# Kernel tuning notes

Hardware: AMD Instinct MI355X
Metric: run time of the kernel (lower is better)

## Reference

```python
import jax, jax.numpy as jnp
import numpy as np
from jax import lax


def _binarize(w):
    # XNOR-style sign binarization: sign(w) with sign(0) -> +1
    return jnp.where(w >= 0, 1.0, -1.0).astype(w.dtype)


def setup_inputs() -> dict:
    key = jax.random.key(0)
    kx, kw = jax.random.split(key)
    X = jax.random.normal(kx, (32, 256, 56, 56), dtype=jnp.float32)   # NCHW
    W = jax.random.normal(kw, (256, 256, 3, 3), dtype=jnp.float32)    # OIHW
    return {"X": X, "W": W}


def reference(X, W):
    Wb = _binarize(W)
    # F.conv2d default: padding=0 (VALID), stride=1
    out = lax.conv_general_dilated(
        X, Wb,
        window_strides=(1, 1),
        padding="VALID",
        dimension_numbers=("NCHW", "OIHW", "NCHW"),
    )
    return out  # [32, 256, 54, 54]
```

## Files before the change

kernel.cpp:

```cpp
#include <hip/hip_runtime.h>
#include <stdint.h>

typedef float f32x4 __attribute__((ext_vector_type(4)));
typedef __bf16 bf16x8 __attribute__((ext_vector_type(8)));
typedef unsigned short u16x8 __attribute__((ext_vector_type(8)));

#define NIMG 32
#define CIN  256
#define HWIN 3136
#define COUT 256
#define HWOUT 2916
#define NPOS 93312

#define XT_BYTES   ((size_t)NIMG*HWIN*CIN*2)
#define WT_OFF     (XT_BYTES + 8192)
#define WT_BYTES   ((size_t)9*4*2*128*64*2)
#define WS_NEED    (WT_OFF + WT_BYTES)

static __device__ __forceinline__ unsigned short f2bf(float f) {
    union { float f; uint32_t u; } v; v.f = f;
    return (unsigned short)((v.u + 0x7FFFu + ((v.u >> 16) & 1u)) >> 16);
}

static __device__ __forceinline__ void gload16(const void* g, void* l) {
    __builtin_amdgcn_global_load_lds(
        (const __attribute__((address_space(1))) void*)g,
        (__attribute__((address_space(3))) void*)l, 16, 0, 0);
}

static __device__ __forceinline__ uint32_t lds_a(const void* p) {
    return (uint32_t)(uintptr_t)(__attribute__((address_space(3))) const void*)p;
}

static __device__ __forceinline__ u16x8 ldsr(uint32_t addr) {
    u16x8 r;
    asm volatile("ds_read_b128 %0, %1" : "=v"(r) : "v"(addr));
    return r;
}

#define BAR()   __builtin_amdgcn_s_barrier()
#define LGKM0() do { asm volatile("s_waitcnt lgkmcnt(0)" ::: "memory"); \
                     __builtin_amdgcn_sched_barrier(0); } while (0)
#define VM2()   asm volatile("s_waitcnt vmcnt(2)" ::: "memory")
#define VM6()   asm volatile("s_waitcnt vmcnt(6)" ::: "memory")
#define VM0()   asm volatile("s_waitcnt vmcnt(0)" ::: "memory")
#define PRIO1() __builtin_amdgcn_s_setprio(1)
#define PRIO0() __builtin_amdgcn_s_setprio(0)

#define MF(a_, b_, c_) __builtin_amdgcn_mfma_f32_16x16x32_bf16( \
    __builtin_bit_cast(bf16x8, a_), __builtin_bit_cast(bf16x8, b_), c_, 0, 0, 0)

#define QUAD(aa, ab, m0_, m1_, c0_, c1_, c2_, c3_)         \
    acc[m0_][0] = MF(aa, c0_, acc[m0_][0]);                \
    acc[m0_][1] = MF(aa, c1_, acc[m0_][1]);                \
    acc[m0_][2] = MF(aa, c2_, acc[m0_][2]);                \
    acc[m0_][3] = MF(aa, c3_, acc[m0_][3]);                \
    acc[m1_][0] = MF(ab, c0_, acc[m1_][0]);                \
    acc[m1_][1] = MF(ab, c1_, acc[m1_][1]);                \
    acc[m1_][2] = MF(ab, c2_, acc[m1_][2]);                \
    acc[m1_][3] = MF(ab, c3_, acc[m1_][3]);

__global__ void wxform(const float* __restrict__ W, unsigned short* __restrict__ Wt) {
    int idx = blockIdx.x * 256 + threadIdx.x;
    int c6 = idx & 63;
    int o7 = (idx >> 6) & 127;
    int ob = (idx >> 13) & 1;
    int cc = (idx >> 14) & 3;
    int k9 = idx >> 16;
    int o = ob * 128 + o7;
    int c = cc * 64 + c6;
    float w = W[(size_t)(o * 256 + c) * 9 + k9];
    Wt[idx] = (w >= 0.0f) ? (unsigned short)0x3F80 : (unsigned short)0xBF80;
}

__global__ void xxform(const float* __restrict__ X, unsigned short* __restrict__ Xt) {
    __shared__ float tile[32][65];
    int bid = blockIdx.x;
    int hwc = bid % 49;
    int cc  = (bid / 49) & 7;
    int n   = bid / (49 * 8);
    int hw0 = hwc * 64;
    int c0  = cc * 32;
    int t = threadIdx.x;
    {
        int c = t >> 3;
        int w = (t & 7) * 8;
        const float* src = X + (size_t)(n * CIN + c0 + c) * HWIN + hw0 + w;
        float4 a = *(const float4*)src;
        float4 b = *(const float4*)(src + 4);
        tile[c][w + 0] = a.x; tile[c][w + 1] = a.y; tile[c][w + 2] = a.z; tile[c][w + 3] = a.w;
        tile[c][w + 4] = b.x; tile[c][w + 5] = b.y; tile[c][w + 6] = b.z; tile[c][w + 7] = b.w;
    }
    __syncthreads();
    {
        int w  = t >> 2;
        int cb = (t & 3) * 8;
        u16x8 v;
        #pragma unroll
        for (int j = 0; j < 8; ++j) v[j] = f2bf(tile[cb + j][w]);
        *(u16x8*)(Xt + (size_t)(n * HWIN + hw0 + w) * 256 + c0 + cb) = v;
    }
}

__global__ __launch_bounds__(512, 2)
void bconv_gemm(const unsigned short* __restrict__ Xt,
                const unsigned short* __restrict__ Wt,
                float* __restrict__ out) {
    __shared__ __align__(16) char smem[98304];

    const int t    = threadIdx.x;
    const int wid  = t >> 6;
    const int lane = t & 63;
    const int l15  = lane & 15;
    const int lg   = lane >> 4;
    const int wr   = wid >> 2;
    const int wc   = wid & 3;
    const int ob   = blockIdx.x;
    const uint32_t P0 = blockIdx.y * 256u;

    const uint32_t colx = (uint32_t)(((t & 7) ^ ((t >> 3) & 7)) << 3);
    const uint32_t aG   = (uint32_t)(t >> 3) * 64u + colx;

    uint32_t base0[4];
    #pragma unroll
    for (int r = 0; r < 4; ++r) {
        uint32_t pos = P0 + (uint32_t)(r * 64 + (t >> 3));
        if (pos >= NPOS) pos = NPOS - 1;
        uint32_t ni = pos / (uint32_t)HWOUT;
        uint32_t rm = pos - ni * HWOUT;
        uint32_t ph = rm / 54u;
        uint32_t pw = rm - ph * 54u;
        base0[r] = ni * HWIN + ph * 56u + pw;
    }

    const uint32_t x7  = (uint32_t)(l15 & 7);
    const uint32_t ck0 = ((((uint32_t)lg) ^ x7) << 4);
    const uint32_t ck1 = (((4u | (uint32_t)lg) ^ x7) << 4);
    const uint32_t ar0 = (uint32_t)(wr * 64 + 0 * 16 + l15) * 128u;
    const uint32_t ar1 = (uint32_t)(wr * 64 + 1 * 16 + l15) * 128u;
    const uint32_t ar2 = (uint32_t)(wr * 64 + 2 * 16 + l15) * 128u;
    const uint32_t ar3 = (uint32_t)(wr * 64 + 3 * 16 + l15) * 128u;
    const uint32_t br0 = 16384u + (uint32_t)(wc * 64 + 0 * 16 + l15) * 128u;
    const uint32_t br1 = 16384u + (uint32_t)(wc * 64 + 1 * 16 + l15) * 128u;
    const uint32_t br2 = 16384u + (uint32_t)(wc * 64 + 2 * 16 + l15) * 128u;
    const uint32_t br3 = 16384u + (uint32_t)(wc * 64 + 3 * 16 + l15) * 128u;

    const uint32_t E = lds_a(smem);
    const uint32_t O = E + 49152u;

    f32x4 acc[4][4];
    #pragma unroll
    for (int m = 0; m < 4; ++m)
        #pragma unroll
        for (int n = 0; n < 4; ++n)
            acc[m][n] = (f32x4){0.f, 0.f, 0.f, 0.f};

    auto STAGE_A = [&](uint32_t bufoff, int kt) {
        int k9 = kt >> 2, cc = kt & 3;
        const unsigned short* p = Wt + ((size_t)(((k9 << 2) | cc) * 2 + ob)) * 8192 + aG;
        gload16(p,        smem + bufoff + (size_t)t * 16);
        gload16(p + 4096, smem + bufoff + 8192 + (size_t)t * 16);
    };
    auto STAGE_B2 = [&](uint32_t bufoff, int kt, int r0) {
        int k9 = kt >> 2, cc = kt & 3;
        int kh = k9 / 3, kw = k9 - kh * 3;
        uint32_t khw = (uint32_t)(kh * 56 + kw);
        #pragma unroll
        for (int r = r0; r < r0 + 2; ++r) {
            const unsigned short* p = Xt + (size_t)(base0[r] + khw) * 256 + (uint32_t)cc * 64u + colx;
            gload16(p, smem + bufoff + 16384 + (size_t)r * 8192 + (size_t)t * 16);
        }
    };

    STAGE_A(0, 0);      STAGE_B2(0, 0, 0);      STAGE_B2(0, 0, 2);
    STAGE_A(49152u, 1); STAGE_B2(49152u, 1, 0); STAGE_B2(49152u, 1, 2);
    VM6();
    BAR();

    u16x8 a00, a01, a10, a11;
    u16x8 b00, b10, b20, b30, b01, b11, b21, b31;

    auto ITER = [&](int kt, bool pf) {
        a00 = ldsr(E + ar0 + ck0); a01 = ldsr(E + ar0 + ck1);
        a10 = ldsr(E + ar1 + ck0); a11 = ldsr(E + ar1 + ck1);
        b00 = ldsr(E + br0 + ck0); b10 = ldsr(E + br1 + ck0);
        b20 = ldsr(E + br2 + ck0); b30 = ldsr(E + br3 + ck0);
        BAR(); LGKM0(); PRIO1();
        QUAD(a00, a10, 0, 1, b00, b10, b20, b30);
        PRIO0(); BAR();
        b01 = ldsr(E + br0 + ck1); b11 = ldsr(E + br1 + ck1);
        b21 = ldsr(E + br2 + ck1); b31 = ldsr(E + br3 + ck1);
        BAR(); LGKM0(); PRIO1();
        QUAD(a01, a11, 0, 1, b01, b11, b21, b31);
        PRIO0(); BAR();
        a00 = ldsr(E + ar2 + ck0); a01 = ldsr(E + ar2 + ck1);
        a10 = ldsr(E + ar3 + ck0); a11 = ldsr(E + ar3 + ck1);
        BAR(); LGKM0(); PRIO1();
        QUAD(a00, a10, 2, 3, b00, b10, b20, b30);
        PRIO0(); BAR();
        if (pf) { STAGE_A(0, kt + 2); VM2(); } else { VM0(); }
        BAR(); PRIO1();
        QUAD(a01, a11, 2, 3, b01, b11, b21, b31);
        PRIO0(); BAR();
        a00 = ldsr(O + ar0 + ck0); a01 = ldsr(O + ar0 + ck1);
        a10 = ldsr(O + ar1 + ck0); a11 = ldsr(O + ar1 + ck1);
        b00 = ldsr(O + br0 + ck0); b10 = ldsr(O + br1 + ck0);
        b20 = ldsr(O + br2 + ck0); b30 = ldsr(O + br3 + ck0);
        if (pf) STAGE_B2(0, kt + 2, 0);
        BAR(); LGKM0(); PRIO1();
        QUAD(a00, a10, 0, 1, b00, b10, b20, b30);
        PRIO0(); BAR();
        b01 = ldsr(O + br0 + ck1); b11 = ldsr(O + br1 + ck1);
        b21 = ldsr(O + br2 + ck1); b31 = ldsr(O + br3 + ck1);
        if (pf) STAGE_B2(0, kt + 2, 2);
        BAR(); LGKM0(); PRIO1();
        QUAD(a01, a11, 0, 1, b01, b11, b21, b31);
        PRIO0(); BAR();
        a00 = ldsr(O + ar2 + ck0); a01 = ldsr(O + ar2 + ck1);
        a10 = ldsr(O + ar3 + ck0); a11 = ldsr(O + ar3 + ck1);
        BAR(); LGKM0(); PRIO1();
        QUAD(a00, a10, 2, 3, b00, b10, b20, b30);
        PRIO0(); BAR();
        if (pf) {
            STAGE_A(49152u, kt + 3);
            STAGE_B2(49152u, kt + 3, 0);
            STAGE_B2(49152u, kt + 3, 2);
            VM6();
        } else {
            VM0();
        }
        BAR(); PRIO1();
        QUAD(a01, a11, 2, 3, b01, b11, b21, b31);
        PRIO0(); BAR();
    };

    for (int kt = 0; kt < 34; kt += 2) ITER(kt, true);
    ITER(34, false);

    const int orow0 = ob * 128 + wr * 64;
    #pragma unroll
    for (int n = 0; n < 4; ++n) {
        uint32_t P = P0 + (uint32_t)(wc * 64 + n * 16 + l15);
        if (P < NPOS) {
            uint32_t ni = P / (uint32_t)HWOUT;
            uint32_t rm = P - ni * HWOUT;
            float* ob_ = out + (size_t)(ni * 256u + orow0) * HWOUT + rm;
            #pragma unroll
            for (int m = 0; m < 4; ++m)
                #pragma unroll
                for (int r = 0; r < 4; ++r)
                    ob_[(size_t)(m * 16 + lg * 4 + r) * HWOUT] = acc[m][n][r];
        }
    }
}

__global__ void bconv_fallback(const float* __restrict__ X, const float* __restrict__ W,
                               float* __restrict__ out) {
    size_t idx = (size_t)blockIdx.x * 256 + threadIdx.x;
    int ow = (int)(idx % 54);
    int oh = (int)((idx / 54) % 54);
    int o  = (int)((idx / 2916) % 256);
    int n  = (int)(idx / 746496);
    float s = 0.f;
    for (int c = 0; c < 256; ++c) {
        const float* xr = X + ((size_t)(n * 256 + c) * 56 + oh) * 56 + ow;
        const float* wr = W + (size_t)(o * 256 + c) * 9;
        #pragma unroll
        for (int kh = 0; kh < 3; ++kh)
            #pragma unroll
            for (int kw = 0; kw < 3; ++kw) {
                float w = wr[kh * 3 + kw];
                float x = xr[kh * 56 + kw];
                s += (w >= 0.f) ? x : -x;
            }
    }
    out[idx] = s;
}

extern "C" void kernel_launch(void* const* d_in, const int* in_sizes, int n_in,
                              void* d_out, int out_size, void* d_ws, size_t ws_size,
                              hipStream_t stream) {
    const float* X = (const float*)d_in[0];
    const float* W = (const float*)d_in[1];
    float* out = (float*)d_out;

    if (ws_size < WS_NEED) {
        bconv_fallback<<<93312, 256, 0, stream>>>(X, W, out);
        return;
    }
    unsigned short* Xt = (unsigned short*)d_ws;
    unsigned short* Wt = (unsigned short*)((char*)d_ws + WT_OFF);

    wxform<<<2304, 256, 0, stream>>>(W, Wt);
    xxform<<<12544, 256, 0, stream>>>(X, Xt);

    dim3 grid(2, 365);
    bconv_gemm<<<grid, 512, 0, stream>>>(Xt, Wt, out);
}
```

Measured before the change: 163.4 us.

## Shrink GEMM block to 128x128 with 4 waves and K-chunk 64

The implicit-GEMM kernel moves from 512-thread blocks on a 128x256 tile to 256-thread blocks on a 128x128 tile, which doubles the grid and lowers LDS use to 64 KB. The inner loop changes from split half-K QUADs to full 16-MFMA steps with 8 fragment reads per step. B addresses are precomputed as byte pointers advanced by an incremental koff. Bounds checks are dropped because NPOS divides evenly by 128. The cost is less reuse per block, more global traffic for the A and B tiles, and a waitcnt schedule that has been changed.

```diff
diff --git a/kernel.cpp b/kernel.cpp
--- a/kernel.cpp
+++ b/kernel.cpp
@@ -14,7 +14,7 @@
 
 #define XT_BYTES   ((size_t)NIMG*HWIN*CIN*2)
 #define WT_OFF     (XT_BYTES + 8192)
-#define WT_BYTES   ((size_t)9*4*2*128*64*2)
+#define WT_BYTES   ((size_t)36*2*128*64*2)
 #define WS_NEED    (WT_OFF + WT_BYTES)
 
 static __device__ __forceinline__ unsigned short f2bf(float f) {
@@ -41,8 +41,7 @@
 #define BAR()   __builtin_amdgcn_s_barrier()
 #define LGKM0() do { asm volatile("s_waitcnt lgkmcnt(0)" ::: "memory"); \
                      __builtin_amdgcn_sched_barrier(0); } while (0)
-#define VM2()   asm volatile("s_waitcnt vmcnt(2)" ::: "memory")
-#define VM6()   asm volatile("s_waitcnt vmcnt(6)" ::: "memory")
+#define VM8()   asm volatile("s_waitcnt vmcnt(8)" ::: "memory")
 #define VM0()   asm volatile("s_waitcnt vmcnt(0)" ::: "memory")
 #define PRIO1() __builtin_amdgcn_s_setprio(1)
 #define PRIO0() __builtin_amdgcn_s_setprio(0)
@@ -50,15 +49,23 @@
 #define MF(a_, b_, c_) __builtin_amdgcn_mfma_f32_16x16x32_bf16( \
     __builtin_bit_cast(bf16x8, a_), __builtin_bit_cast(bf16x8, b_), c_, 0, 0, 0)
 
-#define QUAD(aa, ab, m0_, m1_, c0_, c1_, c2_, c3_)         \
-    acc[m0_][0] = MF(aa, c0_, acc[m0_][0]);                \
-    acc[m0_][1] = MF(aa, c1_, acc[m0_][1]);                \
-    acc[m0_][2] = MF(aa, c2_, acc[m0_][2]);                \
-    acc[m0_][3] = MF(aa, c3_, acc[m0_][3]);                \
-    acc[m1_][0] = MF(ab, c0_, acc[m1_][0]);                \
-    acc[m1_][1] = MF(ab, c1_, acc[m1_][1]);                \
-    acc[m1_][2] = MF(ab, c2_, acc[m1_][2]);                \
-    acc[m1_][3] = MF(ab, c3_, acc[m1_][3]);
+#define M16()                                              \
+    acc[0][0] = MF(a0, b0, acc[0][0]);                     \
+    acc[1][0] = MF(a1, b0, acc[1][0]);                     \
+    acc[2][0] = MF(a2, b0, acc[2][0]);                     \
+    acc[3][0] = MF(a3, b0, acc[3][0]);                     \
+    acc[0][1] = MF(a0, b1, acc[0][1]);                     \
+    acc[1][1] = MF(a1, b1, acc[1][1]);                     \
+    acc[2][1] = MF(a2, b1, acc[2][1]);                     \
+    acc[3][1] = MF(a3, b1, acc[3][1]);                     \
+    acc[0][2] = MF(a0, b2, acc[0][2]);                     \
+    acc[1][2] = MF(a1, b2, acc[1][2]);                     \
+    acc[2][2] = MF(a2, b2, acc[2][2]);                     \
+    acc[3][2] = MF(a3, b2, acc[3][2]);                     \
+    acc[0][3] = MF(a0, b3, acc[0][3]);                     \
+    acc[1][3] = MF(a1, b3, acc[1][3]);                     \
+    acc[2][3] = MF(a2, b3, acc[2][3]);                     \
+    acc[3][3] = MF(a3, b3, acc[3][3]);
 
 __global__ void wxform(const float* __restrict__ W, unsigned short* __restrict__ Wt) {
     int idx = blockIdx.x * 256 + threadIdx.x;
@@ -102,35 +109,36 @@
     }
 }
 
-__global__ __launch_bounds__(512, 2)
+__global__ __launch_bounds__(256, 2)
 void bconv_gemm(const unsigned short* __restrict__ Xt,
                 const unsigned short* __restrict__ Wt,
                 float* __restrict__ out) {
-    __shared__ __align__(16) char smem[98304];
+    __shared__ __align__(16) char smem[65536];
 
     const int t    = threadIdx.x;
     const int wid  = t >> 6;
     const int lane = t & 63;
     const int l15  = lane & 15;
     const int lg   = lane >> 4;
-    const int wr   = wid >> 2;
-    const int wc   = wid & 3;
+    const int wr   = wid >> 1;
+    const int wc   = wid & 1;
     const int ob   = blockIdx.x;
-    const uint32_t P0 = blockIdx.y * 256u;
-
-    const uint32_t colx = (uint32_t)(((t & 7) ^ ((t >> 3) & 7)) << 3);
-    const uint32_t aG   = (uint32_t)(t >> 3) * 64u + colx;
-
-    uint32_t base0[4];
+    const uint32_t P0 = blockIdx.y * 128u;
+
+    const uint32_t colxB = (uint32_t)(((t & 7) ^ ((t >> 3) & 7)) << 4);
+    const uint32_t rowt  = (uint32_t)(t >> 3);
+
+    const char* pA0 = (const char*)Wt + (size_t)ob * 16384 + rowt * 128 + colxB;
+
+    const char* bB[4];
     #pragma unroll
     for (int r = 0; r < 4; ++r) {
-        uint32_t pos = P0 + (uint32_t)(r * 64 + (t >> 3));
-        if (pos >= NPOS) pos = NPOS - 1;
+        uint32_t pos = P0 + (uint32_t)(r * 32) + rowt;
         uint32_t ni = pos / (uint32_t)HWOUT;
         uint32_t rm = pos - ni * HWOUT;
         uint32_t ph = rm / 54u;
         uint32_t pw = rm - ph * 54u;
-        base0[r] = ni * HWIN + ph * 56u + pw;
+        bB[r] = (const char*)Xt + (size_t)(ni * HWIN + ph * 56u + pw) * 512 + colxB;
     }
 
     const uint32_t x7  = (uint32_t)(l15 & 7);
@@ -146,7 +154,7 @@
     const uint32_t br3 = 16384u + (uint32_t)(wc * 64 + 3 * 16 + l15) * 128u;
 
     const uint32_t E = lds_a(smem);
-    const uint32_t O = E + 49152u;
+    const uint32_t O = E + 32768u;
 
     f32x4 acc[4][4];
     #pragma unroll
@@ -156,82 +164,68 @@
             acc[m][n] = (f32x4){0.f, 0.f, 0.f, 0.f};
 
     auto STAGE_A = [&](uint32_t bufoff, int kt) {
-        int k9 = kt >> 2, cc = kt & 3;
-        const unsigned short* p = Wt + ((size_t)(((k9 << 2) | cc) * 2 + ob)) * 8192 + aG;
-        gload16(p,        smem + bufoff + (size_t)t * 16);
-        gload16(p + 4096, smem + bufoff + 8192 + (size_t)t * 16);
-    };
-    auto STAGE_B2 = [&](uint32_t bufoff, int kt, int r0) {
-        int k9 = kt >> 2, cc = kt & 3;
-        int kh = k9 / 3, kw = k9 - kh * 3;
-        uint32_t khw = (uint32_t)(kh * 56 + kw);
-        #pragma unroll
-        for (int r = r0; r < r0 + 2; ++r) {
-            const unsigned short* p = Xt + (size_t)(base0[r] + khw) * 256 + (uint32_t)cc * 64u + colx;
-            gload16(p, smem + bufoff + 16384 + (size_t)r * 8192 + (size_t)t * 16);
+        const char* p = pA0 + (uint32_t)kt * 32768u;
+        #pragma unroll
+        for (int r = 0; r < 4; ++r)
+            gload16(p + r * 4096, smem + bufoff + r * 4096 + (size_t)t * 16);
+    };
+    auto STAGE_B = [&](uint32_t bufoff, uint32_t koff) {
+        #pragma unroll
+        for (int r = 0; r < 4; ++r)
+            gload16(bB[r] + koff, smem + bufoff + 16384 + r * 4096 + (size_t)t * 16);
+    };
+
+    uint32_t ccE = 2, k3E = 0, koffE = 256;
+    uint32_t ccO = 3, k3O = 0, koffO = 384;
+    auto adv2 = [](uint32_t& cc, uint32_t& k3, uint32_t& koff) {
+        #pragma unroll
+        for (int s = 0; s < 2; ++s) {
+            if (cc == 3) { cc = 0; koff += ((k3 == 2) ? 54u : 1u) * 512u - 384u; k3 = (k3 == 2) ? 0u : k3 + 1u; }
+            else         { cc++; koff += 128u; }
         }
     };
 
-    STAGE_A(0, 0);      STAGE_B2(0, 0, 0);      STAGE_B2(0, 0, 2);
-    STAGE_A(49152u, 1); STAGE_B2(49152u, 1, 0); STAGE_B2(49152u, 1, 2);
-    VM6();
+    STAGE_A(0, 0);      STAGE_B(0, 0);
+    STAGE_A(32768u, 1); STAGE_B(32768u, 128);
+    VM8();
     BAR();
 
-    u16x8 a00, a01, a10, a11;
-    u16x8 b00, b10, b20, b30, b01, b11, b21, b31;
+    u16x8 a0, a1, a2, a3, b0, b1, b2, b3;
 
     auto ITER = [&](int kt, bool pf) {
-        a00 = ldsr(E + ar0 + ck0); a01 = ldsr(E + ar0 + ck1);
-        a10 = ldsr(E + ar1 + ck0); a11 = ldsr(E + ar1 + ck1);
-        b00 = ldsr(E + br0 + ck0); b10 = ldsr(E + br1 + ck0);
-        b20 = ldsr(E + br2 + ck0); b30 = ldsr(E + br3 + ck0);
-        BAR(); LGKM0(); PRIO1();
-        QUAD(a00, a10, 0, 1, b00, b10, b20, b30);
-        PRIO0(); BAR();
-        b01 = ldsr(E + br0 + ck1); b11 = ldsr(E + br1 + ck1);
-        b21 = ldsr(E + br2 + ck1); b31 = ldsr(E + br3 + ck1);
-        BAR(); LGKM0(); PRIO1();
-        QUAD(a01, a11, 0, 1, b01, b11, b21, b31);
-        PRIO0(); BAR();
-        a00 = ldsr(E + ar2 + ck0); a01 = ldsr(E + ar2 + ck1);
-        a10 = ldsr(E + ar3 + ck0); a11 = ldsr(E + ar3 + ck1);
-        BAR(); LGKM0(); PRIO1();
-        QUAD(a00, a10, 2, 3, b00, b10, b20, b30);
-        PRIO0(); BAR();
-        if (pf) { STAGE_A(0, kt + 2); VM2(); } else { VM0(); }
-        BAR(); PRIO1();
-        QUAD(a01, a11, 2, 3, b01, b11, b21, b31);
-        PRIO0(); BAR();
-        a00 = ldsr(O + ar0 + ck0); a01 = ldsr(O + ar0 + ck1);
-        a10 = ldsr(O + ar1 + ck0); a11 = ldsr(O + ar1 + ck1);
-        b00 = ldsr(O + br0 + ck0); b10 = ldsr(O + br1 + ck0);
-        b20 = ldsr(O + br2 + ck0); b30 = ldsr(O + br3 + ck0);
-        if (pf) STAGE_B2(0, kt + 2, 0);
-        BAR(); LGKM0(); PRIO1();
-        QUAD(a00, a10, 0, 1, b00, b10, b20, b30);
-        PRIO0(); BAR();
-        b01 = ldsr(O + br0 + ck1); b11 = ldsr(O + br1 + ck1);
-        b21 = ldsr(O + br2 + ck1); b31 = ldsr(O + br3 + ck1);
-        if (pf) STAGE_B2(0, kt + 2, 2);
-        BAR(); LGKM0(); PRIO1();
-        QUAD(a01, a11, 0, 1, b01, b11, b21, b31);
-        PRIO0(); BAR();
-        a00 = ldsr(O + ar2 + ck0); a01 = ldsr(O + ar2 + ck1);
-        a10 = ldsr(O + ar3 + ck0); a11 = ldsr(O + ar3 + ck1);
-        BAR(); LGKM0(); PRIO1();
-        QUAD(a00, a10, 2, 3, b00, b10, b20, b30);
-        PRIO0(); BAR();
-        if (pf) {
-            STAGE_A(49152u, kt + 3);
-            STAGE_B2(49152u, kt + 3, 0);
-            STAGE_B2(49152u, kt + 3, 2);
-            VM6();
-        } else {
-            VM0();
-        }
-        BAR(); PRIO1();
-        QUAD(a01, a11, 2, 3, b01, b11, b21, b31);
-        PRIO0(); BAR();
+        a0 = ldsr(E + ar0 + ck0); a1 = ldsr(E + ar1 + ck0);
+        a2 = ldsr(E + ar2 + ck0); a3 = ldsr(E + ar3 + ck0);
+        b0 = ldsr(E + br0 + ck0); b1 = ldsr(E + br1 + ck0);
+        b2 = ldsr(E + br2 + ck0); b3 = ldsr(E + br3 + ck0);
+        BAR(); LGKM0(); PRIO1();
+        M16();
+        PRIO0(); BAR();
+        a0 = ldsr(E + ar0 + ck1); a1 = ldsr(E + ar1 + ck1);
+        a2 = ldsr(E + ar2 + ck1); a3 = ldsr(E + ar3 + ck1);
+        b0 = ldsr(E + br0 + ck1); b1 = ldsr(E + br1 + ck1);
+        b2 = ldsr(E + br2 + ck1); b3 = ldsr(E + br3 + ck1);
+        VM0();
+        BAR(); LGKM0(); PRIO1();
+        M16();
+        PRIO0(); BAR();
+        a0 = ldsr(O + ar0 + ck0); a1 = ldsr(O + ar1 + ck0);
+        a2 = ldsr(O + ar2 + ck0); a3 = ldsr(O + ar3 + ck0);
+        b0 = ldsr(O + br0 + ck0); b1 = ldsr(O + br1 + ck0);
+        b2 = ldsr(O + br2 + ck0); b3 = ldsr(O + br3 + ck0);
+        if (pf) { STAGE_A(0, kt + 2); STAGE_B(0, koffE); }
+        BAR(); LGKM0(); PRIO1();
+        M16();
+        PRIO0(); BAR();
+        a0 = ldsr(O + ar0 + ck1); a1 = ldsr(O + ar1 + ck1);
+        a2 = ldsr(O + ar2 + ck1); a3 = ldsr(O + ar3 + ck1);
+        b0 = ldsr(O + br0 + ck1); b1 = ldsr(O + br1 + ck1);
+        b2 = ldsr(O + br2 + ck1); b3 = ldsr(O + br3 + ck1);
+        if (pf) { STAGE_A(32768u, kt + 3); STAGE_B(32768u, koffO); VM8(); }
+        else    { VM0(); }
+        BAR(); LGKM0(); PRIO1();
+        M16();
+        PRIO0(); BAR();
+        if (pf) { adv2(ccE, k3E, koffE); adv2(ccO, k3O, koffO); }
     };
 
     for (int kt = 0; kt < 34; kt += 2) ITER(kt, true);
@@ -241,16 +235,14 @@
     #pragma unroll
     for (int n = 0; n < 4; ++n) {
         uint32_t P = P0 + (uint32_t)(wc * 64 + n * 16 + l15);
-        if (P < NPOS) {
-            uint32_t ni = P / (uint32_t)HWOUT;
-            uint32_t rm = P - ni * HWOUT;
-            float* ob_ = out + (size_t)(ni * 256u + orow0) * HWOUT + rm;
+        uint32_t ni = P / (uint32_t)HWOUT;
+        uint32_t rm = P - ni * HWOUT;
+        float* ob_ = out + (size_t)(ni * 256u + orow0) * HWOUT + rm;
+        #pragma unroll
+        for (int m = 0; m < 4; ++m)
             #pragma unroll
-            for (int m = 0; m < 4; ++m)
-                #pragma unroll
-                for (int r = 0; r < 4; ++r)
-                    ob_[(size_t)(m * 16 + lg * 4 + r) * HWOUT] = acc[m][n][r];
-        }
+            for (int r = 0; r < 4; ++r)
+                ob_[(size_t)(m * 16 + lg * 4 + r) * HWOUT] = acc[m][n][r];
     }
 }
 
@@ -294,6 +286,6 @@
     wxform<<<2304, 256, 0, stream>>>(W, Wt);
     xxform<<<12544, 256, 0, stream>>>(X, Xt);
 
-    dim3 grid(2, 365);
-    bconv_gemm<<<grid, 512, 0, stream>>>(Xt, Wt, out);
-}
+    dim3 grid(2, 729);
+    bconv_gemm<<<grid, 256, 0, stream>>>(Xt, Wt, out);
+}
```

Result: faster. 147.0 us (-10.0%).
